# Kernel tuning notes

Measured on AMD Instinct MI355X. Metric: run time of the kernel, lower is better.

The kernel has to match this reference:

```python
import jax, jax.numpy as jnp
from jax import lax
import numpy as np

OUT_H, OUT_W = 8, 32
SCALE = 4.0
B, CIN, COUT, H, W = 4, 256, 128, 256, 256
N_PER_IMG = 32
N_ROIS = B * N_PER_IMG


def setup_inputs() -> dict:
    key = jax.random.key(0)
    k = jax.random.split(key, 6)
    feats = jax.random.normal(k[0], (B, CIN, H, W), jnp.float32)
    rng = np.random.default_rng(0)
    # rois sorted by batch index so output ordering matches the torch double loop
    bidx = np.repeat(np.arange(B), N_PER_IMG).astype(np.float32)
    x1 = rng.uniform(0, W * SCALE * 0.6, N_ROIS)
    y1 = rng.uniform(0, H * SCALE * 0.6, N_ROIS)
    bw = rng.uniform(48, W * SCALE * 0.35, N_ROIS)
    bh = rng.uniform(32, H * SCALE * 0.25, N_ROIS)
    rois = jnp.asarray(np.stack([bidx, x1, y1, x1 + bw, y1 + bh], 1), jnp.float32)
    # rescaled per-ROI bitmap masks at feature resolution (values 0/1)
    masks = (jax.random.uniform(k[1], (N_ROIS, H, W)) > 0.5).astype(jnp.float32)
    conv_w = jax.random.normal(k[2], (COUT, CIN, 3, 3), jnp.float32) * 0.02
    conv_b = jnp.zeros((COUT,), jnp.float32)
    bn_gamma = jnp.ones((COUT,), jnp.float32)
    bn_beta = jnp.zeros((COUT,), jnp.float32)
    bn_mean = jax.random.normal(k[3], (COUT,), jnp.float32) * 0.1
    bn_var = jax.random.uniform(k[4], (COUT,), jnp.float32, 0.5, 1.5)
    return dict(feats=feats, rois=rois, masks=masks, conv_w=conv_w, conv_b=conv_b,
                bn_gamma=bn_gamma, bn_beta=bn_beta, bn_mean=bn_mean, bn_var=bn_var)


def _forward(feats, rois, masks, conv_w, conv_b, bn_gamma, bn_beta, bn_mean, bn_var):
    # conv3x3(pad=1) + BN(eval) + ReLU
    feat = lax.conv_general_dilated(feats, conv_w, (1, 1), 'SAME',
                                    dimension_numbers=('NCHW', 'OIHW', 'NCHW'))
    feat = feat + conv_b[None, :, None, None]
    scale = (bn_gamma / jnp.sqrt(bn_var + 1e-5))[None, :, None, None]
    feat = (feat - bn_mean[None, :, None, None]) * scale + bn_beta[None, :, None, None]
    feat = jax.nn.relu(feat)
    Hf, Wf = feat.shape[2], feat.shape[3]

    pad = jnp.array([-1.0, -1.0, 1.0, 1.0], jnp.float32)
    # torch .long() truncates toward zero; astype(int32) matches for these values
    boxes = (rois[:, 1:] / SCALE + pad).astype(jnp.int32)
    l = jnp.clip(boxes[:, 0], 0, Wf)
    t = jnp.clip(boxes[:, 1], 0, Hf)
    r = jnp.clip(boxes[:, 2], 0, Wf)
    b = jnp.clip(boxes[:, 3], 0, Hf)
    bi = rois[:, 0].astype(jnp.int32)

    ii = jnp.arange(OUT_H, dtype=jnp.float32) + 0.5
    jj = jnp.arange(OUT_W, dtype=jnp.float32) + 0.5

    def one_roi(bi_r, l_r, t_r, r_r, b_r, mask_r):
        ch = (b_r - t_r).astype(jnp.float32)
        cw = (r_r - l_r).astype(jnp.float32)
        transpose = ch > 1.5 * cw  # tall crops get transposed before resize
        ones_row = jnp.ones((1, OUT_W), jnp.float32)
        ones_col = jnp.ones((OUT_H, 1), jnp.float32)
        # source coords (align_corners=False): (dst+0.5)*src/dst_size - 0.5
        V = jnp.where(transpose,
                      (jj * ch / OUT_W - 0.5)[None, :] * ones_col,
                      (ii * ch / OUT_H - 0.5)[:, None] * ones_row)
        U = jnp.where(transpose,
                      (ii * cw / OUT_H - 0.5)[:, None] * ones_row,
                      (jj * cw / OUT_W - 0.5)[None, :] * ones_col)
        V = jnp.maximum(V, 0.0)
        U = jnp.maximum(U, 0.0)
        chi = jnp.maximum(b_r - t_r, 1)
        cwi = jnp.maximum(r_r - l_r, 1)
        vf = jnp.floor(V)
        uf = jnp.floor(U)
        y0 = jnp.minimum(vf.astype(jnp.int32), chi - 1)
        y1 = jnp.minimum(y0 + 1, chi - 1)
        x0 = jnp.minimum(uf.astype(jnp.int32), cwi - 1)
        x1 = jnp.minimum(x0 + 1, cwi - 1)
        wy = V - vf
        wx = U - uf
        ay0 = jnp.clip(t_r + y0, 0, Hf - 1)
        ay1 = jnp.clip(t_r + y1, 0, Hf - 1)
        ax0 = jnp.clip(l_r + x0, 0, Wf - 1)
        ax1 = jnp.clip(l_r + x1, 0, Wf - 1)

        def samp(ay, ax):
            v = feat[bi_r, :, ay, ax]  # (OUT_H, OUT_W, C) gather
            return jnp.moveaxis(v, -1, 0) * mask_r[ay, ax][None]  # (C, OUT_H, OUT_W)

        out = (((1 - wy) * (1 - wx))[None] * samp(ay0, ax0)
               + ((1 - wy) * wx)[None] * samp(ay0, ax1)
               + (wy * (1 - wx))[None] * samp(ay1, ax0)
               + (wy * wx)[None] * samp(ay1, ax1))
        valid = jnp.logical_and(r_r > l_r, b_r > t_r)
        return jnp.where(valid, out, 0.0)

    return jax.vmap(one_roi)(bi, l, t, r, b, masks)  # (N, C, OUT_H, OUT_W)


def reference(feats, rois, masks, conv_w, conv_b, bn_gamma, bn_beta, bn_mean, bn_var):
    return _forward(feats, rois, masks, conv_w, conv_b, bn_gamma, bn_beta, bn_mean, bn_var)
```

## Files before the change

### kernel.cpp

```cpp
#include <hip/hip_runtime.h>

typedef __attribute__((ext_vector_type(8))) short short8;
typedef __attribute__((ext_vector_type(4))) float float4v;

static __device__ __forceinline__ unsigned short f2bf(float x) {
    unsigned u = __float_as_uint(x);
    return (unsigned short)((u + 0x7fffu + ((u >> 16) & 1u)) >> 16);
}
static __device__ __forceinline__ int imin(int a, int b) { return a < b ? a : b; }
static __device__ __forceinline__ int imax(int a, int b) { return a > b ? a : b; }

static __device__ __forceinline__ void gload_lds16(const void* g, void* l) {
    __builtin_amdgcn_global_load_lds(
        (const __attribute__((address_space(1))) void*)g,
        (__attribute__((address_space(3))) void*)l, 16, 0, 0);
}

#define FB16_IMG 16777216ull
#define FCL_IMG   8388608ull
#define FEAT_IMG 16777216ull

__global__ void wprep_kernel(const float* __restrict__ conv_w,
                             unsigned short* __restrict__ wprep,
                             unsigned short* __restrict__ zguard) {
    if (blockIdx.x == 0 && threadIdx.x < 32) zguard[threadIdx.x] = 0;
    int e = blockIdx.x * 256 + threadIdx.x;
    if (e >= 294912) return;
    int ci = e & 31;
    int t2 = e >> 5;
    int co = t2 & 127;
    int t3 = t2 >> 7;
    int tap = t3 % 9;
    int chunk = t3 / 9;
    int cin = chunk * 32 + ci;
    int ty = tap / 3, tx = tap - ty * 3;
    wprep[e] = f2bf(conv_w[((co * 256 + cin) * 3 + ty) * 3 + tx]);
}

__global__ __launch_bounds__(256) void prep_kernel(const float* __restrict__ feats,
                                                   unsigned short* __restrict__ fb16) {
    const int bx = blockIdx.x;
    const int b  = bx >> 11;
    const int r  = bx & 2047;
    const int chunk = r >> 8;
    const int h = r & 255;
    const int w = threadIdx.x;
    const float* src = feats + (size_t)b * FEAT_IMG
                     + ((size_t)(chunk * 32) * 256 + h) * 256 + w;
    union { unsigned short u16[32]; short8 v8[4]; } p;
#pragma unroll
    for (int ci = 0; ci < 32; ++ci)
        p.u16[ci] = f2bf(src[(size_t)ci * 65536]);
    unsigned short* dst = fb16 + (size_t)b * FB16_IMG
                        + ((size_t)(chunk * 256 + h) * 256 + w) * 32;
#pragma unroll
    for (int k = 0; k < 4; ++k)
        *(short8*)(dst + k * 8) = p.v8[k];
}

__global__ __launch_bounds__(256, 2) void conv_bn_relu_kernel(
    const unsigned short* __restrict__ fb16_all,
    const float* __restrict__ conv_b,
    const float* __restrict__ bn_gamma,
    const float* __restrict__ bn_beta,
    const float* __restrict__ bn_mean,
    const float* __restrict__ bn_var,
    const unsigned short* __restrict__ wprep,
    const unsigned short* __restrict__ zguard,
    unsigned short* __restrict__ feat_cl_all) {

    __shared__ __align__(16) unsigned short in_lds[6 * 34 * 32];
    __shared__ float aL[128], bL[128];

    const int tid = threadIdx.x;
    const int b   = blockIdx.x >> 9;
    const int rem = blockIdx.x & 511;
    const int h0  = (rem >> 3) * 4;
    const int w0  = (rem & 7) * 32;

    const unsigned short* fb16 = fb16_all + (size_t)b * FB16_IMG;
    unsigned short* feat_cl_b  = feat_cl_all + (size_t)b * FCL_IMG;

    if (tid < 128) {
        float s = bn_gamma[tid] * rsqrtf(bn_var[tid] + 1e-5f);
        aL[tid] = s;
        bL[tid] = (conv_b[tid] - bn_mean[tid]) * s + bn_beta[tid];
    }

    const int wave = tid >> 6;
    const int lane = tid & 63;
    const int q    = lane >> 4;
    const int l15  = lane & 15;

    long off_s[4];
    int  lds_s[4];
    bool oob_s[4];
#pragma unroll
    for (int i = 0; i < 4; ++i) {
        int u = wave * 204 + i * 64 + lane;
        int row = u / 136;
        int r2  = u - row * 136;
        int col = r2 >> 2;
        int part = r2 & 3;
        int gh = h0 - 1 + row;
        int gw = w0 - 1 + col;
        oob_s[i] = ((unsigned)gh > 255u) || ((unsigned)gw > 255u);
        off_s[i] = (long)(gh * 256 + gw) * 32 + part * 8;
        lds_s[i] = u * 8;
    }

    float4v acc[2][8];
#pragma unroll
    for (int a = 0; a < 2; ++a)
#pragma unroll
        for (int p = 0; p < 8; ++p)
            acc[a][p] = (float4v){0.f, 0.f, 0.f, 0.f};

    for (int chunk = 0; chunk < 8; ++chunk) {
        const unsigned short* fb = fb16 + (size_t)chunk * (65536u * 32u);
#pragma unroll
        for (int i = 0; i < 3; ++i) {
            const unsigned short* gp = oob_s[i] ? zguard : (fb + off_s[i]);
            gload_lds16(gp, &in_lds[lds_s[i]]);
        }
        if (lane < 12) {
            const unsigned short* gp = oob_s[3] ? zguard : (fb + off_s[3]);
            gload_lds16(gp, &in_lds[lds_s[3]]);
        }
        __syncthreads();

#pragma unroll
        for (int tap = 0; tap < 9; ++tap) {
            const int dy = tap / 3, dx = tap - dy * 3;
            const short8* wpt = (const short8*)wprep + (chunk * 9 + tap) * 512;
            short8 a0 = wpt[(wave * 32 + l15) * 4 + q];
            short8 a1 = wpt[(wave * 32 + 16 + l15) * 4 + q];
#pragma unroll
            for (int pt = 0; pt < 8; ++pt) {
                const int r  = pt >> 1;
                const int c0 = (pt & 1) * 16;
                short8 bf = *(const short8*)&in_lds[((r + dy) * 34 + (c0 + l15 + dx)) * 32 + q * 8];
                acc[0][pt] = __builtin_amdgcn_mfma_f32_16x16x32_bf16(a0, bf, acc[0][pt], 0, 0, 0);
                acc[1][pt] = __builtin_amdgcn_mfma_f32_16x16x32_bf16(a1, bf, acc[1][pt], 0, 0, 0);
            }
        }
        __syncthreads();
    }

#pragma unroll
    for (int ct = 0; ct < 2; ++ct) {
        const int coutb = wave * 32 + ct * 16 + q * 4;
        const float s0 = aL[coutb + 0], s1 = aL[coutb + 1];
        const float s2 = aL[coutb + 2], s3 = aL[coutb + 3];
        const float o0 = bL[coutb + 0], o1 = bL[coutb + 1];
        const float o2 = bL[coutb + 2], o3 = bL[coutb + 3];
#pragma unroll
        for (int pt = 0; pt < 8; ++pt) {
            const int r  = pt >> 1;
            const int cl = (pt & 1) * 16 + l15;
            float4v v = acc[ct][pt];
            unsigned short p0 = f2bf(fmaxf(v[0] * s0 + o0, 0.f));
            unsigned short p1 = f2bf(fmaxf(v[1] * s1 + o1, 0.f));
            unsigned short p2 = f2bf(fmaxf(v[2] * s2 + o2, 0.f));
            unsigned short p3 = f2bf(fmaxf(v[3] * s3 + o3, 0.f));
            unsigned long long pk = (unsigned long long)p0
                                  | ((unsigned long long)p1 << 16)
                                  | ((unsigned long long)p2 << 32)
                                  | ((unsigned long long)p3 << 48);
            size_t off = ((size_t)((h0 + r) * 256 + (w0 + cl))) * 128 + coutb;
            *(unsigned long long*)(feat_cl_b + off) = pk;
        }
    }
}

__global__ __launch_bounds__(256) void roi_gather_kernel(
    const float* __restrict__ rois,
    const float* __restrict__ masks,
    const unsigned long long* __restrict__ feat_u64,
    float* __restrict__ out) {

    __shared__ int   offs[64][4];
    __shared__ float wts[64][4];

    const int blk = blockIdx.x;
    const int roi = blk >> 2;
    const int q0  = blk & 3;
    const int tid = threadIdx.x;

    const float* rp = rois + roi * 5;
    const int bi = (int)rp[0];
    int l_ = (int)(rp[1] * 0.25f - 1.0f);
    int t_ = (int)(rp[2] * 0.25f - 1.0f);
    int r_ = (int)(rp[3] * 0.25f + 1.0f);
    int b_ = (int)(rp[4] * 0.25f + 1.0f);
    l_ = imin(imax(l_, 0), 256); t_ = imin(imax(t_, 0), 256);
    r_ = imin(imax(r_, 0), 256); b_ = imin(imax(b_, 0), 256);
    const float ch = (float)(b_ - t_);
    const float cw = (float)(r_ - l_);
    const bool transpose = ch > 1.5f * cw;
    const int chi = imax(b_ - t_, 1);
    const int cwi = imax(r_ - l_, 1);
    const float vscale = ((r_ > l_) && (b_ > t_)) ? 1.f : 0.f;

    {
        const int pos_l  = tid >> 2;
        const int corner = tid & 3;
        const int pos = q0 * 64 + pos_l;
        const int i = pos >> 5, j = pos & 31;
        const float fi = (float)i + 0.5f, fj = (float)j + 0.5f;
        float V = transpose ? (fj * ch * (1.f / 32.f) - 0.5f)
                            : (fi * ch * (1.f / 8.f)  - 0.5f);
        float U = transpose ? (fi * cw * (1.f / 8.f)  - 0.5f)
                            : (fj * cw * (1.f / 32.f) - 0.5f);
        V = fmaxf(V, 0.f); U = fmaxf(U, 0.f);
        float vf = floorf(V), uf = floorf(U);
        int y0 = imin((int)vf, chi - 1); int y1 = imin(y0 + 1, chi - 1);
        int x0 = imin((int)uf, cwi - 1); int x1 = imin(x0 + 1, cwi - 1);
        float wy = V - vf, wx = U - uf;
        int ay = imin(imax(t_ + ((corner & 2) ? y1 : y0), 0), 255);
        int ax = imin(imax(l_ + ((corner & 1) ? x1 : x0), 0), 255);
        float wgt = ((corner & 2) ? wy : (1.f - wy)) * ((corner & 1) ? wx : (1.f - wx));
        wts[pos_l][corner]  = wgt * masks[(size_t)roi * 65536 + ay * 256 + ax] * vscale;
        offs[pos_l][corner] = (ay * 256 + ax) * 32;
    }
    __syncthreads();

    const int cq = tid & 31;
    const int pq = tid >> 5;
    const unsigned long long* fb = feat_u64 + (size_t)bi * (65536ull * 32ull) + cq;
    float* op = out + (size_t)roi * 32768 + (size_t)cq * 4 * 256 + q0 * 64;

#pragma unroll 2
    for (int po = 0; po < 8; ++po) {
        const int pos_l = po * 8 + pq;
        float a0 = 0.f, a1 = 0.f, a2 = 0.f, a3 = 0.f;
#pragma unroll
        for (int k = 0; k < 4; ++k) {
            unsigned long long u = fb[offs[pos_l][k]];
            float w = wts[pos_l][k];
            a0 += w * __uint_as_float((unsigned)(u)       << 16);
            a1 += w * __uint_as_float((unsigned)(u >> 16) << 16);
            a2 += w * __uint_as_float((unsigned)(u >> 32) << 16);
            a3 += w * __uint_as_float((unsigned)(u >> 48) << 16);
        }
        op[pos_l]       = a0;
        op[pos_l + 256] = a1;
        op[pos_l + 512] = a2;
        op[pos_l + 768] = a3;
    }
}

extern "C" void kernel_launch(void* const* d_in, const int* in_sizes, int n_in,
                              void* d_out, int out_size, void* d_ws, size_t ws_size,
                              hipStream_t stream) {
    const float* feats    = (const float*)d_in[0];
    const float* rois     = (const float*)d_in[1];
    const float* masks    = (const float*)d_in[2];
    const float* conv_w   = (const float*)d_in[3];
    const float* conv_b   = (const float*)d_in[4];
    const float* bn_gamma = (const float*)d_in[5];
    const float* bn_beta  = (const float*)d_in[6];
    const float* bn_mean  = (const float*)d_in[7];
    const float* bn_var   = (const float*)d_in[8];
    float* out = (float*)d_out;

    unsigned short* wprep   = (unsigned short*)d_ws;
    unsigned short* zguard  = (unsigned short*)((char*)d_ws + 0x90000);
    unsigned short* feat_cl = (unsigned short*)((char*)d_ws + (1ull << 20));
    unsigned short* fb16    = (unsigned short*)((char*)d_ws + (1ull << 20) + (64ull << 20));

    const size_t need_merged = (1ull << 20) + (64ull << 20) + (128ull << 20);

    hipLaunchKernelGGL(wprep_kernel, dim3(1152), dim3(256), 0, stream,
                       conv_w, wprep, zguard);

    if (ws_size >= need_merged) {
        hipLaunchKernelGGL(prep_kernel, dim3(8192), dim3(256), 0, stream,
                           feats, fb16);
        hipLaunchKernelGGL(conv_bn_relu_kernel, dim3(2048), dim3(256), 0, stream,
                           fb16, conv_b, bn_gamma, bn_beta, bn_mean, bn_var,
                           wprep, zguard, feat_cl);
    } else {
        for (int b = 0; b < 4; ++b) {
            hipLaunchKernelGGL(prep_kernel, dim3(2048), dim3(256), 0, stream,
                               feats + (size_t)b * FEAT_IMG, fb16);
            hipLaunchKernelGGL(conv_bn_relu_kernel, dim3(512), dim3(256), 0, stream,
                               fb16, conv_b, bn_gamma, bn_beta, bn_mean, bn_var,
                               wprep, zguard, feat_cl + (size_t)b * FCL_IMG);
        }
    }

    hipLaunchKernelGGL(roi_gather_kernel, dim3(512), dim3(256), 0, stream,
                       rois, masks, (const unsigned long long*)feat_cl, out);
}
```

Measured before the change: 577.9 us.

## Double-buffer conv input tiles and re-layout bf16 features per 8-channel slab

The bf16 feature buffer now stores each 32-channel chunk as four 8-channel slabs instead of 32 interleaved channels per pixel. The prep kernel reads float4 vectors along width instead of scalar strided loads. The conv kernel double-buffers its LDS input tile so the next chunk's global-to-LDS loads overlap the current chunk's MFMA work, and raises the launch-bounds occupancy hint from 2 to 3. This aims to hide load latency and coalesce the prep reads, at the cost of twice the LDS and more register pressure.

```diff
diff --git a/kernel.cpp b/kernel.cpp
--- a/kernel.cpp
+++ b/kernel.cpp
@@ -2,6 +2,7 @@
 
 typedef __attribute__((ext_vector_type(8))) short short8;
 typedef __attribute__((ext_vector_type(4))) float float4v;
+typedef __attribute__((ext_vector_type(4))) float f32x4;
 
 static __device__ __forceinline__ unsigned short f2bf(float x) {
     unsigned u = __float_as_uint(x);
@@ -19,6 +20,8 @@
 #define FB16_IMG 16777216ull
 #define FCL_IMG   8388608ull
 #define FEAT_IMG 16777216ull
+#define CHUNK_STRIDE 2097152
+#define Q_STRIDE      524288
 
 __global__ void wprep_kernel(const float* __restrict__ conv_w,
                              unsigned short* __restrict__ wprep,
@@ -44,21 +47,31 @@
     const int r  = bx & 2047;
     const int chunk = r >> 8;
     const int h = r & 255;
-    const int w = threadIdx.x;
+    const int t = threadIdx.x;
+    const int q  = t >> 6;
+    const int w4 = (t & 63) * 4;
+
     const float* src = feats + (size_t)b * FEAT_IMG
-                     + ((size_t)(chunk * 32) * 256 + h) * 256 + w;
-    union { unsigned short u16[32]; short8 v8[4]; } p;
-#pragma unroll
-    for (int ci = 0; ci < 32; ++ci)
-        p.u16[ci] = f2bf(src[(size_t)ci * 65536]);
+                     + (size_t)(chunk * 32 + q * 8) * 65536 + h * 256 + w4;
+    f32x4 v[8];
+#pragma unroll
+    for (int k = 0; k < 8; ++k)
+        v[k] = *(const f32x4*)(src + (size_t)k * 65536);
+
     unsigned short* dst = fb16 + (size_t)b * FB16_IMG
-                        + ((size_t)(chunk * 256 + h) * 256 + w) * 32;
-#pragma unroll
-    for (int k = 0; k < 4; ++k)
-        *(short8*)(dst + k * 8) = p.v8[k];
-}
-
-__global__ __launch_bounds__(256, 2) void conv_bn_relu_kernel(
+                        + (size_t)chunk * CHUNK_STRIDE + (size_t)q * Q_STRIDE
+                        + ((size_t)h * 256 + w4) * 8;
+#pragma unroll
+    for (int j = 0; j < 4; ++j) {
+        short8 o;
+#pragma unroll
+        for (int k = 0; k < 8; ++k)
+            o[k] = (short)f2bf(v[k][j]);
+        *(short8*)(dst + j * 8) = o;
+    }
+}
+
+__global__ __launch_bounds__(256, 3) void conv_bn_relu_kernel(
     const unsigned short* __restrict__ fb16_all,
     const float* __restrict__ conv_b,
     const float* __restrict__ bn_gamma,
@@ -69,7 +82,7 @@
     const unsigned short* __restrict__ zguard,
     unsigned short* __restrict__ feat_cl_all) {
 
-    __shared__ __align__(16) unsigned short in_lds[6 * 34 * 32];
+    __shared__ __align__(16) unsigned short in_lds[2][6528];
     __shared__ float aL[128], bL[128];
 
     const int tid = threadIdx.x;
@@ -97,16 +110,14 @@
     bool oob_s[4];
 #pragma unroll
     for (int i = 0; i < 4; ++i) {
-        int u = wave * 204 + i * 64 + lane;
-        int row = u / 136;
-        int r2  = u - row * 136;
-        int col = r2 >> 2;
-        int part = r2 & 3;
+        int rem_u = i * 64 + lane;
+        int row = rem_u / 34;
+        int col = rem_u - row * 34;
         int gh = h0 - 1 + row;
         int gw = w0 - 1 + col;
         oob_s[i] = ((unsigned)gh > 255u) || ((unsigned)gw > 255u);
-        off_s[i] = (long)(gh * 256 + gw) * 32 + part * 8;
-        lds_s[i] = u * 8;
+        off_s[i] = (long)wave * Q_STRIDE + (long)(gh * 256 + gw) * 8;
+        lds_s[i] = (wave * 204 + rem_u) * 8;
     }
 
     float4v acc[2][8];
@@ -116,30 +127,48 @@
         for (int p = 0; p < 8; ++p)
             acc[a][p] = (float4v){0.f, 0.f, 0.f, 0.f};
 
-    for (int chunk = 0; chunk < 8; ++chunk) {
-        const unsigned short* fb = fb16 + (size_t)chunk * (65536u * 32u);
+    {
+        const unsigned short* fb = fb16;
 #pragma unroll
         for (int i = 0; i < 3; ++i) {
             const unsigned short* gp = oob_s[i] ? zguard : (fb + off_s[i]);
-            gload_lds16(gp, &in_lds[lds_s[i]]);
+            gload_lds16(gp, &in_lds[0][lds_s[i]]);
         }
         if (lane < 12) {
             const unsigned short* gp = oob_s[3] ? zguard : (fb + off_s[3]);
-            gload_lds16(gp, &in_lds[lds_s[3]]);
-        }
-        __syncthreads();
+            gload_lds16(gp, &in_lds[0][lds_s[3]]);
+        }
+    }
+    __syncthreads();
+
+    for (int c = 0; c < 8; ++c) {
+        const int buf = c & 1;
+
+        if (c < 7) {
+            const unsigned short* fb = fb16 + (size_t)(c + 1) * CHUNK_STRIDE;
+#pragma unroll
+            for (int i = 0; i < 3; ++i) {
+                const unsigned short* gp = oob_s[i] ? zguard : (fb + off_s[i]);
+                gload_lds16(gp, &in_lds[buf ^ 1][lds_s[i]]);
+            }
+            if (lane < 12) {
+                const unsigned short* gp = oob_s[3] ? zguard : (fb + off_s[3]);
+                gload_lds16(gp, &in_lds[buf ^ 1][lds_s[3]]);
+            }
+        }
 
 #pragma unroll
         for (int tap = 0; tap < 9; ++tap) {
             const int dy = tap / 3, dx = tap - dy * 3;
-            const short8* wpt = (const short8*)wprep + (chunk * 9 + tap) * 512;
+            const short8* wpt = (const short8*)wprep + (c * 9 + tap) * 512;
             short8 a0 = wpt[(wave * 32 + l15) * 4 + q];
             short8 a1 = wpt[(wave * 32 + 16 + l15) * 4 + q];
 #pragma unroll
             for (int pt = 0; pt < 8; ++pt) {
                 const int r  = pt >> 1;
                 const int c0 = (pt & 1) * 16;
-                short8 bf = *(const short8*)&in_lds[((r + dy) * 34 + (c0 + l15 + dx)) * 32 + q * 8];
+                short8 bf = *(const short8*)
+                    &in_lds[buf][((q * 6 + r + dy) * 34 + (c0 + l15 + dx)) * 8];
                 acc[0][pt] = __builtin_amdgcn_mfma_f32_16x16x32_bf16(a0, bf, acc[0][pt], 0, 0, 0);
                 acc[1][pt] = __builtin_amdgcn_mfma_f32_16x16x32_bf16(a1, bf, acc[1][pt], 0, 0, 0);
             }
```

After: 665.2 us. 15.1% more time.

## Enlarge conv tile to 8 rows and vectorize bf16 prep transpose

Applied to the files above, without the earlier changes.

The conv kernel now computes an 8x32 output tile per block instead of 4x32, with a 10-row halo in LDS and 16 accumulator tiles per output-channel group. Each block reuses weights over twice the pixels and the halo overhead per pixel drops, at the cost of more accumulator registers and fewer blocks. The prep kernel now reads float4 vectors and writes four pixels per thread with 16-byte stores, aiming for better memory coalescing.

```diff
diff --git a/kernel.cpp b/kernel.cpp
--- a/kernel.cpp
+++ b/kernel.cpp
@@ -2,6 +2,7 @@
 
 typedef __attribute__((ext_vector_type(8))) short short8;
 typedef __attribute__((ext_vector_type(4))) float float4v;
+typedef __attribute__((ext_vector_type(4))) float f32x4;
 
 static __device__ __forceinline__ unsigned short f2bf(float x) {
     unsigned u = __float_as_uint(x);
@@ -19,6 +20,7 @@
 #define FB16_IMG 16777216ull
 #define FCL_IMG   8388608ull
 #define FEAT_IMG 16777216ull
+#define CHUNK_STRIDE 2097152
 
 __global__ void wprep_kernel(const float* __restrict__ conv_w,
                              unsigned short* __restrict__ wprep,
@@ -40,22 +42,34 @@
 __global__ __launch_bounds__(256) void prep_kernel(const float* __restrict__ feats,
                                                    unsigned short* __restrict__ fb16) {
     const int bx = blockIdx.x;
-    const int b  = bx >> 11;
-    const int r  = bx & 2047;
-    const int chunk = r >> 8;
-    const int h = r & 255;
-    const int w = threadIdx.x;
+    const int b  = bx >> 9;
+    const int r  = bx & 511;
+    const int chunk = r >> 6;
+    const int hg = r & 63;
+    const int t = threadIdx.x;
+    const int h  = hg * 4 + (t >> 6);
+    const int w4 = (t & 63) * 4;
+
     const float* src = feats + (size_t)b * FEAT_IMG
-                     + ((size_t)(chunk * 32) * 256 + h) * 256 + w;
-    union { unsigned short u16[32]; short8 v8[4]; } p;
-#pragma unroll
-    for (int ci = 0; ci < 32; ++ci)
-        p.u16[ci] = f2bf(src[(size_t)ci * 65536]);
+                     + (size_t)(chunk * 32) * 65536 + h * 256 + w4;
     unsigned short* dst = fb16 + (size_t)b * FB16_IMG
-                        + ((size_t)(chunk * 256 + h) * 256 + w) * 32;
-#pragma unroll
-    for (int k = 0; k < 4; ++k)
-        *(short8*)(dst + k * 8) = p.v8[k];
+                        + (size_t)chunk * CHUNK_STRIDE
+                        + ((size_t)h * 256 + w4) * 32;
+#pragma unroll
+    for (int qq = 0; qq < 4; ++qq) {
+        f32x4 v[8];
+#pragma unroll
+        for (int k = 0; k < 8; ++k)
+            v[k] = *(const f32x4*)(src + (size_t)(qq * 8 + k) * 65536);
+#pragma unroll
+        for (int j = 0; j < 4; ++j) {
+            short8 o;
+#pragma unroll
+            for (int k = 0; k < 8; ++k)
+                o[k] = (short)f2bf(v[k][j]);
+            *(short8*)(dst + j * 32 + qq * 8) = o;
+        }
+    }
 }
 
 __global__ __launch_bounds__(256, 2) void conv_bn_relu_kernel(
@@ -69,13 +83,13 @@
     const unsigned short* __restrict__ zguard,
     unsigned short* __restrict__ feat_cl_all) {
 
-    __shared__ __align__(16) unsigned short in_lds[6 * 34 * 32];
+    __shared__ __align__(16) unsigned short in_lds[10 * 34 * 32];
     __shared__ float aL[128], bL[128];
 
     const int tid = threadIdx.x;
-    const int b   = blockIdx.x >> 9;
-    const int rem = blockIdx.x & 511;
-    const int h0  = (rem >> 3) * 4;
+    const int b   = blockIdx.x >> 8;
+    const int rem = blockIdx.x & 255;
+    const int h0  = (rem >> 3) * 8;
     const int w0  = (rem & 7) * 32;
 
     const unsigned short* fb16 = fb16_all + (size_t)b * FB16_IMG;
@@ -92,12 +106,12 @@
     const int q    = lane >> 4;
     const int l15  = lane & 15;
 
-    long off_s[4];
-    int  lds_s[4];
-    bool oob_s[4];
-#pragma unroll
-    for (int i = 0; i < 4; ++i) {
-        int u = wave * 204 + i * 64 + lane;
+    int  off_s[6];
+    int  lds_s[6];
+    bool oob_s[6];
+#pragma unroll
+    for (int i = 0; i < 6; ++i) {
+        int u = wave * 340 + i * 64 + lane;
         int row = u / 136;
         int r2  = u - row * 136;
         int col = r2 >> 2;
@@ -105,41 +119,42 @@
         int gh = h0 - 1 + row;
         int gw = w0 - 1 + col;
         oob_s[i] = ((unsigned)gh > 255u) || ((unsigned)gw > 255u);
-        off_s[i] = (long)(gh * 256 + gw) * 32 + part * 8;
+        off_s[i] = (gh * 256 + gw) * 32 + part * 8;
         lds_s[i] = u * 8;
     }
 
-    float4v acc[2][8];
+    float4v acc[2][16];
 #pragma unroll
     for (int a = 0; a < 2; ++a)
 #pragma unroll
-        for (int p = 0; p < 8; ++p)
+        for (int p = 0; p < 16; ++p)
             acc[a][p] = (float4v){0.f, 0.f, 0.f, 0.f};
 
-    for (int chunk = 0; chunk < 8; ++chunk) {
-        const unsigned short* fb = fb16 + (size_t)chunk * (65536u * 32u);
-#pragma unroll
-        for (int i = 0; i < 3; ++i) {
+    for (int c = 0; c < 8; ++c) {
+        const unsigned short* fb = fb16 + (size_t)c * CHUNK_STRIDE;
+#pragma unroll
+        for (int i = 0; i < 5; ++i) {
             const unsigned short* gp = oob_s[i] ? zguard : (fb + off_s[i]);
             gload_lds16(gp, &in_lds[lds_s[i]]);
         }
-        if (lane < 12) {
-            const unsigned short* gp = oob_s[3] ? zguard : (fb + off_s[3]);
-            gload_lds16(gp, &in_lds[lds_s[3]]);
+        if (lane < 20) {
+            const unsigned short* gp = oob_s[5] ? zguard : (fb + off_s[5]);
+            gload_lds16(gp, &in_lds[lds_s[5]]);
         }
         __syncthreads();
 
 #pragma unroll
         for (int tap = 0; tap < 9; ++tap) {
             const int dy = tap / 3, dx = tap - dy * 3;
-            const short8* wpt = (const short8*)wprep + (chunk * 9 + tap) * 512;
+            const short8* wpt = (const short8*)wprep + (c * 9 + tap) * 512;
             short8 a0 = wpt[(wave * 32 + l15) * 4 + q];
             short8 a1 = wpt[(wave * 32 + 16 + l15) * 4 + q];
 #pragma unroll
-            for (int pt = 0; pt < 8; ++pt) {
+            for (int pt = 0; pt < 16; ++pt) {
                 const int r  = pt >> 1;
                 const int c0 = (pt & 1) * 16;
-                short8 bf = *(const short8*)&in_lds[((r + dy) * 34 + (c0 + l15 + dx)) * 32 + q * 8];
+                short8 bf = *(const short8*)
+                    &in_lds[((r + dy) * 34 + (c0 + l15 + dx)) * 32 + q * 8];
                 acc[0][pt] = __builtin_amdgcn_mfma_f32_16x16x32_bf16(a0, bf, acc[0][pt], 0, 0, 0);
                 acc[1][pt] = __builtin_amdgcn_mfma_f32_16x16x32_bf16(a1, bf, acc[1][pt], 0, 0, 0);
             }
@@ -155,7 +170,7 @@
         const float o0 = bL[coutb + 0], o1 = bL[coutb + 1];
         const float o2 = bL[coutb + 2], o3 = bL[coutb + 3];
 #pragma unroll
-        for (int pt = 0; pt < 8; ++pt) {
+        for (int pt = 0; pt < 16; ++pt) {
             const int r  = pt >> 1;
             const int cl = (pt & 1) * 16 + l15;
             float4v v = acc[ct][pt];
@@ -275,16 +290,16 @@
                        conv_w, wprep, zguard);
 
     if (ws_size >= need_merged) {
-        hipLaunchKernelGGL(prep_kernel, dim3(8192), dim3(256), 0, stream,
+        hipLaunchKernelGGL(prep_kernel, dim3(2048), dim3(256), 0, stream,
                            feats, fb16);
-        hipLaunchKernelGGL(conv_bn_relu_kernel, dim3(2048), dim3(256), 0, stream,
+        hipLaunchKernelGGL(conv_bn_relu_kernel, dim3(1024), dim3(256), 0, stream,
                            fb16, conv_b, bn_gamma, bn_beta, bn_mean, bn_var,
                            wprep, zguard, feat_cl);
     } else {
         for (int b = 0; b < 4; ++b) {
-            hipLaunchKernelGGL(prep_kernel, dim3(2048), dim3(256), 0, stream,
+            hipLaunchKernelGGL(prep_kernel, dim3(512), dim3(256), 0, stream,
                                feats + (size_t)b * FEAT_IMG, fb16);
-            hipLaunchKernelGGL(conv_bn_relu_kernel, dim3(512), dim3(256), 0, stream,
+            hipLaunchKernelGGL(conv_bn_relu_kernel, dim3(256), dim3(256), 0, stream,
                                fb16, conv_b, bn_gamma, bn_beta, bn_mean, bn_var,
                                wprep, zguard, feat_cl + (size_t)b * FCL_IMG);
         }
```

Result: slower. 955.8 us (+65.4%).
